# Optimization experiments

Hardware: AMD Instinct MI355X
Metric: run time of the kernel (lower is better)

The kernel has to match this reference:

```python
import jax, jax.numpy as jnp
import numpy as np

N = 32768      # nodes
E = 262144     # edges (avg degree 8)
F = 64         # channels per irrep
Z = 10         # species
R = 8          # radial basis size
H = 64         # radial MLP hidden
P_TP = 5       # TP paths: 0x0->0, 0x1->1, 1x0->1, 1x1->0, 1x1->1
P_SC = 9       # symmetric-contraction paths up to correlation 3
EPS = 0.25     # epsilon ~ 1/sqrt(avg_num_neighbors)


def _split(x):
    # [N, 4F] -> scalars [N,F], vectors [N,F,3] (irreps F x (0e + 1o))
    return x[:, :F], x[:, F:].reshape(x.shape[0], F, 3)


def _merge(s, v):
    return jnp.concatenate([s, v.reshape(v.shape[0], 3 * F)], axis=-1)


def _lin(s, v, Ws, Wv):
    # irreps-wise linear (separate channel mixing per l), fan-in normalized
    inv = 1.0 / np.sqrt(F)
    return (s @ Ws) * inv, jnp.einsum('nfc,fg->ngc', v, Wv) * inv


def _linZ(s, v, Ws, Wv, species):
    # per-species indexed linear, extra 1/sqrt(num_species) as in linZ
    inv = 1.0 / np.sqrt(F * Z)
    return (jnp.einsum('nf,nfg->ng', s, Ws[species]) * inv,
            jnp.einsum('nfc,nfg->ngc', v, Wv[species]) * inv)


def setup_inputs() -> dict:
    key = jax.random.key(0)
    ks = jax.random.split(key, 24)
    f32 = jnp.float32
    return {
        'vectors': jax.random.normal(ks[0], (E, 3), f32),
        'node_feats': jax.random.normal(ks[1], (N, 4 * F), f32),
        'radial_embeddings': jax.random.normal(ks[2], (E, R), f32),
        'W_skip_s': jax.random.normal(ks[3], (Z, F, F), f32),
        'W_skip_v': jax.random.normal(ks[4], (Z, F, F), f32),
        'W_up_s': jax.random.normal(ks[5], (F, F), f32),
        'W_up_v': jax.random.normal(ks[6], (F, F), f32),
        'W_mlp1': jax.random.normal(ks[7], (R, H), f32),
        'W_mlp2': jax.random.normal(ks[8], (H, H), f32),
        'W_mlp3': jax.random.normal(ks[9], (H, H), f32),
        'W_mlp4': jax.random.normal(ks[10], (H, P_TP * F), f32),
        'W_down_s': jax.random.normal(ks[11], (F, F), f32),
        'W_down_v': jax.random.normal(ks[12], (F, F), f32),
        'W_sc': jax.random.normal(ks[13], (Z, P_SC, F), f32),
        'W_post_s': jax.random.normal(ks[14], (F, F), f32),
        'W_post_v': jax.random.normal(ks[15], (F, F), f32),
        'W_out': jax.random.normal(ks[16], (F, 1), f32),
        'node_species': jax.random.randint(ks[17], (N,), 0, Z),
        'senders': jax.random.randint(ks[18], (E,), 0, N),
        'receivers': jax.random.randint(ks[19], (E,), 0, N),
    }


def reference(vectors, node_feats, radial_embeddings, W_skip_s, W_skip_v,
              W_up_s, W_up_v, W_mlp1, W_mlp2, W_mlp3, W_mlp4,
              W_down_s, W_down_v, W_sc, W_post_s, W_post_v, W_out,
              node_species, senders, receivers):
    s, v = _split(node_feats)

    # self connection: per-species skip linear (linZ_skip_tp)
    skip_s, skip_v = _linZ(s, v, W_skip_s, W_skip_v, node_species)

    # linear_up
    s, v = _lin(s, v, W_up_s, W_up_v)

    # spherical harmonics of edge vectors (l=0 is constant, l=1 = unit vector)
    Y1 = vectors / (jnp.linalg.norm(vectors, axis=-1, keepdims=True) + 1e-9)  # [E,3]

    # radial MLP (64,64,64,P_TP*F), no bias, fan-in normalized, silu
    act = jax.nn.silu
    h = act(radial_embeddings @ W_mlp1 * (1.0 / np.sqrt(R)))
    h = act(h @ W_mlp2 * (1.0 / np.sqrt(H)))
    h = act(h @ W_mlp3 * (1.0 / np.sqrt(H)))
    w = (h @ W_mlp4 * (1.0 / np.sqrt(H))).reshape(E, P_TP, F)  # per-edge path weights

    # channelwise tensor product: gather senders, CG-couple with Y, scatter to receivers
    ss = s[senders]              # [E,F]
    vv = v[senders]              # [E,F,3]
    dot = jnp.einsum('efc,ec->ef', vv, Y1)        # 1x1 -> 0
    cross = jnp.cross(vv, Y1[:, None, :])         # 1x1 -> 1
    m_s = w[:, 0] * ss + w[:, 3] * dot
    m_v = (w[:, 1][..., None] * Y1[:, None, :]
           + w[:, 2][..., None] * vv
           + w[:, 4][..., None] * cross * (1.0 / np.sqrt(2.0)))
    s = jax.ops.segment_sum(m_s * EPS, receivers, num_segments=N)  # [N,F]
    v = jax.ops.segment_sum(m_v * EPS, receivers, num_segments=N)  # [N,F,3]

    # linear_down
    s, v = _lin(s, v, W_down_s, W_down_v)

    # per-species symmetric contraction, correlation orders 1..3
    wz = W_sc[node_species]             # [N,P_SC,F]
    vn2 = jnp.sum(v * v, axis=-1)       # [N,F] invariant |v|^2
    s_out = (wz[:, 0] * s + wz[:, 1] * s * s + wz[:, 2] * vn2
             + wz[:, 3] * s ** 3 + wz[:, 4] * s * vn2)
    v_out = (wz[:, 5] + wz[:, 6] * s + wz[:, 7] * s * s + wz[:, 8] * vn2)[..., None] * v

    # linear_post_sc + skip connection
    s, v = _lin(s_out, v_out, W_post_s, W_post_v)
    s = s + skip_s
    v = v + skip_v

    # linear_readout to scalar output irreps (0e)
    node_outputs = s @ W_out * (1.0 / np.sqrt(F))  # [N,1]
    return node_outputs, _merge(s, v)
```

## Files before the change

### kernel.cpp

```cpp
#include <hip/hip_runtime.h>
#include <math.h>


#define NN 32768
#define EE 262144
#define EC 131072
#define ZZ 10
#define NB 128
#define NT_MAX 2064
#define INV8 0.125f
#define INV_SQRT8 0.35355339059327373f
#define INVZ 0.039528470752104741f
#define EPS_C 0.25f
#define RS2 0.70710678118654752f

typedef _Float16 f16;
typedef f16 f16x8 __attribute__((ext_vector_type(8)));
typedef f16 f16x4 __attribute__((ext_vector_type(4)));
typedef f16 f16x2 __attribute__((ext_vector_type(2)));
typedef float f32x4 __attribute__((ext_vector_type(4)));

#define LDFRAG(fid) (*(const f16x8*)(fragw + ((size_t)(fid) << 9) + (lane << 3)))

__device__ __forceinline__ unsigned bfpair(float lo, float hi) {
  unsigned ul = __float_as_uint(lo);
  unsigned uh = __float_as_uint(hi);
  ul = (ul + 0x7FFFu + ((ul >> 16) & 1u)) >> 16;
  uh = (uh + 0x7FFFu + ((uh >> 16) & 1u)) >> 16;
  return ul | (uh << 16);
}

__device__ __forceinline__ unsigned short f2h(float x) {
  union { f16 h; unsigned short u; } cv;
  cv.h = (f16)x;
  return cv.u;
}

__device__ __forceinline__ f16x8 pack8(float4 a, float4 b) {
  f16x8 r;
  r[0] = (f16)a.x; r[1] = (f16)a.y; r[2] = (f16)a.z; r[3] = (f16)a.w;
  r[4] = (f16)b.x; r[5] = (f16)b.y; r[6] = (f16)b.z; r[7] = (f16)b.w;
  return r;
}

__device__ __forceinline__ float silu_f(float x) {
  return x / (1.0f + __expf(-x));
}

__global__ __launch_bounds__(256) void k_frag(
    const float* __restrict__ W1, const float* __restrict__ W2,
    const float* __restrict__ W3, const float* __restrict__ W4,
    const float* __restrict__ Wdns, const float* __restrict__ Wdnv,
    const float* __restrict__ Wpss, const float* __restrict__ Wpsv,
    const float* __restrict__ Wsks, const float* __restrict__ Wskv,
    const float* __restrict__ Wups, const float* __restrict__ Wupv,
    unsigned short* __restrict__ fragw) {
  int id = blockIdx.x * 256 + threadIdx.x;
  if (id >= 268 * 64) return;
  int fid = id >> 6, lane = id & 63;
  int q = lane >> 4, c = lane & 15;
  const float* W; int K = 64, N = 64, t, ks; float sc; int w4 = 0;
  if (fid < 4)       { W = W1; K = 8; N = 64; t = fid; ks = 0; sc = INV_SQRT8; }
  else if (fid < 12) { W = W2; t = (fid - 4) >> 1;  ks = (fid - 4) & 1;  sc = INV8; }
  else if (fid < 20) { W = W3; t = (fid - 12) >> 1; ks = (fid - 12) & 1; sc = INV8; }
  else if (fid < 60) { W = W4; N = 320; t = (fid - 20) >> 1; ks = (fid - 20) & 1; sc = INV8; w4 = 1; }
  else {
    int f2 = fid - 60; sc = INV8;
    if (f2 < 8)        { W = Wdns; }
    else if (f2 < 16)  { W = Wdnv; f2 -= 8; }
    else if (f2 < 24)  { W = Wpss; f2 -= 16; }
    else if (f2 < 32)  { W = Wpsv; f2 -= 24; }
    else if (f2 < 112) { f2 -= 32; W = Wsks + (f2 >> 3) * 4096; f2 &= 7; sc = INVZ; }
    else if (f2 < 192) { f2 -= 112; W = Wskv + (f2 >> 3) * 4096; f2 &= 7; sc = INVZ; }
    else if (f2 < 200) { W = Wups; f2 -= 192; }
    else               { W = Wupv; f2 -= 200; }
    t = f2 >> 1; ks = f2 & 1;
  }
  int col = w4 ? ((t % 5) * 64 + 4 * c + (t / 5)) : (t * 16 + c);
  unsigned short o[8];
#pragma unroll
  for (int i = 0; i < 8; ++i) {
    int k = ks * 32 + 8 * q + i;
    float v = (k < K) ? W[k * N + col] * sc : 0.0f;
    o[i] = f2h(v);
  }
  *(uint4*)(fragw + (size_t)id * 8) = *(const uint4*)o;
}

__global__ __launch_bounds__(256) void k_hist(const int* __restrict__ rcv,
                                              int* __restrict__ cnt) {
  int e = blockIdx.x * 256 + threadIdx.x;
  atomicAdd(&cnt[rcv[e]], 1);
}

__global__ __launch_bounds__(1024) void k_scan(const int* __restrict__ cnt,
                                               int* __restrict__ row_start,
                                               int* __restrict__ cursor) {
  __shared__ int tot[1024];
  int t = threadIdx.x;
  int base = t * 32;
  int local[32];
  int s = 0;
#pragma unroll
  for (int i = 0; i < 32; ++i) { local[i] = s; s += cnt[base + i]; }
  tot[t] = s;
  __syncthreads();
  for (int off = 1; off < 1024; off <<= 1) {
    int v = (t >= off) ? tot[t - off] : 0;
    __syncthreads();
    tot[t] += v;
    __syncthreads();
  }
  int prefix = (t == 0) ? 0 : tot[t - 1];
#pragma unroll
  for (int i = 0; i < 32; ++i) {
    int v = prefix + local[i];
    row_start[base + i] = v;
    cursor[base + i] = v;
  }
  if (t == 1023) row_start[NN] = prefix + s;
}

__global__ __launch_bounds__(256) void k_fill(const int* __restrict__ rcv,
                                              int* __restrict__ cursor,
                                              int* __restrict__ elist) {
  int e = blockIdx.x * 256 + threadIdx.x;
  int pos = atomicAdd(&cursor[rcv[e]], 1);
  elist[pos] = e;
}

__global__ __launch_bounds__(256) void k_nhist(const int* __restrict__ species,
                                               int* __restrict__ sbins,
                                               int* __restrict__ bcnt) {
  __shared__ int h[ZZ];
  int t = threadIdx.x;
  if (t < ZZ) h[t] = 0;
  __syncthreads();
  int n = blockIdx.x * 256 + t;
  atomicAdd(&h[species[n]], 1);
  __syncthreads();
  if (t < ZZ) {
    bcnt[blockIdx.x * ZZ + t] = h[t];
    atomicAdd(&sbins[32 + t], h[t]);
  }
}

__global__ __launch_bounds__(256) void k_nscan(int* __restrict__ sbins,
                                               const int* __restrict__ bcnt,
                                               int* __restrict__ bbase,
                                               int* __restrict__ tspec) {
  __shared__ int sb[12];
  int t = threadIdx.x;
  if (t == 0) {
    int off = 0;
    for (int z = 0; z < ZZ; ++z) {
      sb[z] = off;
      off += ((sbins[32 + z] + 15) >> 4) << 4;
    }
    sb[ZZ] = off;
  }
  __syncthreads();
  if (t < ZZ) {
    int run = sb[t];
    for (int b = 0; b < NB; ++b) {
      bbase[b * ZZ + t] = run;
      run += bcnt[b * ZZ + t];
    }
  }
  for (int i = t; i < NT_MAX; i += 256) {
    int base = i * 16, z = -1;
#pragma unroll
    for (int zz = 0; zz < ZZ; ++zz)
      if (base >= sb[zz] && base < sb[zz + 1]) z = zz;
    tspec[i] = z;
  }
}

__global__ __launch_bounds__(256) void k_nfill(const int* __restrict__ species,
                                               const int* __restrict__ bbase,
                                               int* __restrict__ nperm) {
  __shared__ int cur[ZZ];
  int t = threadIdx.x;
  if (t < ZZ) cur[t] = bbase[blockIdx.x * ZZ + t];
  __syncthreads();
  int n = blockIdx.x * 256 + t;
  int pos = atomicAdd(&cur[species[n]], 1);
  nperm[pos] = n;
}

__global__ __launch_bounds__(256) void k_up2(
    const float* __restrict__ nf,
    const unsigned short* __restrict__ fragw,
    unsigned short* __restrict__ s_up, unsigned short* __restrict__ v_up) {
  int lane = threadIdx.x & 63;
  int wv = threadIdx.x >> 6;
  int n0 = (blockIdx.x * 4 + wv) * 16;
  int q = lane >> 4, c = lane & 15;
  const f32x4 zero4 = {0.f, 0.f, 0.f, 0.f};
  const float* nrow = nf + (size_t)(n0 + c) * 256;

  f16x8 aS[2], aX[2], aY[2], aZ[2];
#pragma unroll
  for (int ks = 0; ks < 2; ++ks) {
    int k0 = ks * 32 + 8 * q;
    aS[ks] = pack8(*(const float4*)(nrow + k0), *(const float4*)(nrow + k0 + 4));
    float vb[24];
    const float4* vp = (const float4*)(nrow + 64 + 3 * k0);
#pragma unroll
    for (int j = 0; j < 6; ++j) *(float4*)(vb + 4 * j) = vp[j];
#pragma unroll
    for (int i = 0; i < 8; ++i) {
      aX[ks][i] = (f16)vb[3 * i];
      aY[ks][i] = (f16)vb[3 * i + 1];
      aZ[ks][i] = (f16)vb[3 * i + 2];
    }
  }

  f32x4 os[4], ox[4], oy[4], oz[4];
#pragma unroll
  for (int t = 0; t < 4; ++t)
#pragma unroll
    for (int ks = 0; ks < 2; ++ks) {
      f16x8 bS = LDFRAG(252 + t * 2 + ks);
      f16x8 bV = LDFRAG(260 + t * 2 + ks);
      os[t] = __builtin_amdgcn_mfma_f32_16x16x32_f16(aS[ks], bS, ks ? os[t] : zero4, 0, 0, 0);
      ox[t] = __builtin_amdgcn_mfma_f32_16x16x32_f16(aX[ks], bV, ks ? ox[t] : zero4, 0, 0, 0);
      oy[t] = __builtin_amdgcn_mfma_f32_16x16x32_f16(aY[ks], bV, ks ? oy[t] : zero4, 0, 0, 0);
      oz[t] = __builtin_amdgcn_mfma_f32_16x16x32_f16(aZ[ks], bV, ks ? oz[t] : zero4, 0, 0, 0);
    }

#pragma unroll
  for (int t = 0; t < 4; ++t)
#pragma unroll
    for (int r = 0; r < 4; ++r) {
      int n = n0 + 4 * q + r;
      int ch = 16 * t + c;
      s_up[n * 64 + ch] = f2h(os[t][r]);
      v_up[(n * 3 + 0) * 64 + ch] = f2h(ox[t][r]);
      v_up[(n * 3 + 1) * 64 + ch] = f2h(oy[t][r]);
      v_up[(n * 3 + 2) * 64 + ch] = f2h(oz[t][r]);
    }
}

__global__ __launch_bounds__(256, 4) void k_mlp(
    const float* __restrict__ re, const int* __restrict__ elist,
    const float* __restrict__ vecs, const int* __restrict__ snd,
    const unsigned short* __restrict__ fragw,
    const unsigned short* __restrict__ s_up,
    const unsigned short* __restrict__ v_up,
    unsigned short* __restrict__ wm, int ip0) {
  __shared__ float hs[4][1088];
  int lane = threadIdx.x & 63;
  int wv = threadIdx.x >> 6;
  int q = lane >> 4, c = lane & 15;
  int ipb = ip0 + (blockIdx.x * 4 + wv) * 16;
  float* hw = hs[wv];
  const f32x4 zero4 = {0.f, 0.f, 0.f, 0.f};

  f16x8 a1 = {0, 0, 0, 0, 0, 0, 0, 0};
  if (q == 0) {
    int e = elist[ipb + c];
    const float4* rp = (const float4*)(re + (size_t)e * 8);
    a1 = pack8(rp[0], rp[1]);
  }
  {
    f32x4 acc[4];
#pragma unroll
    for (int t = 0; t < 4; ++t)
      acc[t] = __builtin_amdgcn_mfma_f32_16x16x32_f16(a1, LDFRAG(t), zero4, 0, 0, 0);
#pragma unroll
    for (int t = 0; t < 4; ++t)
#pragma unroll
      for (int r = 0; r < 4; ++r) {
        float x = silu_f(acc[t][r]);
        hw[(4 * q + r) * 68 + ((16 * t + c) ^ (r << 3))] = x;
      }
  }

#pragma unroll
  for (int L = 0; L < 2; ++L) {
    int base = 4 + 8 * L;
    f16x8 af0, af1;
    {
      const float* hp = hw + c * 68 + 8 * (q ^ (c & 3));
      af0 = pack8(*(const float4*)hp, *(const float4*)(hp + 4));
      af1 = pack8(*(const float4*)(hp + 32), *(const float4*)(hp + 36));
    }
    f32x4 acc[4];
#pragma unroll
    for (int t = 0; t < 4; ++t) {
      acc[t] = __builtin_amdgcn_mfma_f32_16x16x32_f16(af0, LDFRAG(base + t * 2), zero4, 0, 0, 0);
      acc[t] = __builtin_amdgcn_mfma_f32_16x16x32_f16(af1, LDFRAG(base + t * 2 + 1), acc[t], 0, 0, 0);
    }
#pragma unroll
    for (int t = 0; t < 4; ++t)
#pragma unroll
      for (int r = 0; r < 4; ++r) {
        float x = silu_f(acc[t][r]);
        hw[(4 * q + r) * 68 + ((16 * t + c) ^ (r << 3))] = x;
      }
  }

  f16x8 a4k0, a4k1;
  {
    const float* hp = hw + c * 68 + 8 * (q ^ (c & 3));
    a4k0 = pack8(*(const float4*)hp, *(const float4*)(hp + 4));
    a4k1 = pack8(*(const float4*)(hp + 32), *(const float4*)(hp + 36));
  }

  int se_[4];
  float Yx[4], Yy[4], Yz[4];
#pragma unroll
  for (int r = 0; r < 4; ++r) {
    int e = elist[ipb + 4 * q + r];
    float ex = vecs[(size_t)e * 3 + 0];
    float ey = vecs[(size_t)e * 3 + 1];
    float ez = vecs[(size_t)e * 3 + 2];
    float rn = 1.0f / (sqrtf(ex * ex + ey * ey + ez * ez) + 1e-9f);
    Yx[r] = ex * rn; Yy[r] = ey * rn; Yz[r] = ez * rn;
    se_[r] = snd[e];
  }

  size_t orow = (size_t)(ipb - ip0);
#pragma unroll 1
  for (int pg = 0; pg < 2; ++pg) {
    f16x2 gs[4], gx[4], gy[4], gz[4];
#pragma unroll
    for (int r = 0; r < 4; ++r) {
      const unsigned short* sr = s_up + (size_t)se_[r] * 64 + 4 * c + 2 * pg;
      const unsigned short* vr = v_up + (size_t)se_[r] * 192 + 4 * c + 2 * pg;
      gs[r] = *(const f16x2*)sr;
      gx[r] = *(const f16x2*)vr;
      gy[r] = *(const f16x2*)(vr + 64);
      gz[r] = *(const f16x2*)(vr + 128);
    }
    float pms[4], pmx[4], pmy[4], pmz[4];
#pragma unroll
    for (int ig2 = 0; ig2 < 2; ++ig2) {
      int ig = 2 * pg + ig2;
      f32x4 o[5];
#pragma unroll
      for (int p = 0; p < 5; ++p) {
        o[p] = __builtin_amdgcn_mfma_f32_16x16x32_f16(
            a4k0, LDFRAG(20 + (ig * 5 + p) * 2 + 0), zero4, 0, 0, 0);
        o[p] = __builtin_amdgcn_mfma_f32_16x16x32_f16(
            a4k1, LDFRAG(20 + (ig * 5 + p) * 2 + 1), o[p], 0, 0, 0);
      }
#pragma unroll
      for (int r = 0; r < 4; ++r) {
        float ss = (float)gs[r][ig2];
        float vx = (float)gx[r][ig2], vy = (float)gy[r][ig2], vz = (float)gz[r][ig2];
        float dt = vx * Yx[r] + vy * Yy[r] + vz * Yz[r];
        float cx = vy * Yz[r] - vz * Yy[r];
        float cy = vz * Yx[r] - vx * Yz[r];
        float cz = vx * Yy[r] - vy * Yx[r];
        float ms = EPS_C * (o[0][r] * ss + o[3][r] * dt);
        float mx = EPS_C * (o[1][r] * Yx[r] + o[2][r] * vx + o[4][r] * (cx * RS2));
        float my = EPS_C * (o[1][r] * Yy[r] + o[2][r] * vy + o[4][r] * (cy * RS2));
        float mz = EPS_C * (o[1][r] * Yz[r] + o[2][r] * vz + o[4][r] * (cz * RS2));
        if (ig2 == 0) {
          pms[r] = ms; pmx[r] = mx; pmy[r] = my; pmz[r] = mz;
        } else {
          unsigned short* wr = wm + (orow + 4 * q + r) * 256 + 4 * c + 2 * pg;
          *(unsigned*)(wr)       = bfpair(pms[r], ms);
          *(unsigned*)(wr + 64)  = bfpair(pmx[r], mx);
          *(unsigned*)(wr + 128) = bfpair(pmy[r], my);
          *(unsigned*)(wr + 192) = bfpair(pmz[r], mz);
        }
      }
    }
  }
}

__global__ __launch_bounds__(256) void k_gather(
    const unsigned short* __restrict__ m_buf,
    const int* __restrict__ row_start,
    float* __restrict__ acc, int e0, int e1) {
  int g = threadIdx.x & 63;
  int wv = threadIdx.x >> 6;
  int n = blockIdx.x * 4 + wv;
  int beg = row_start[n], end = row_start[n + 1];
  int lo = beg > e0 ? beg : e0;
  int hi = end < e1 ? end : e1;
  if (lo >= hi) return;
  float4 a = make_float4(0.f, 0.f, 0.f, 0.f);
  for (int i = lo; i < hi; ++i) {
    uint2 m = *(const uint2*)(m_buf + (size_t)(i - e0) * 256 + g * 4);
    a.x += __uint_as_float(m.x << 16);
    a.y += __uint_as_float(m.x & 0xFFFF0000u);
    a.z += __uint_as_float(m.y << 16);
    a.w += __uint_as_float(m.y & 0xFFFF0000u);
  }
  float* dst = acc + (size_t)n * 256 + g * 4;
  float4 p = *(const float4*)dst;
  *(float4*)dst = make_float4(a.x + p.x, a.y + p.y, a.z + p.z, a.w + p.w);
}

__global__ __launch_bounds__(128) void k_post2(
    const float* __restrict__ nf, const float* __restrict__ acc,
    const unsigned short* __restrict__ fragw,
    const float* __restrict__ Wsc, const float* __restrict__ Wout,
    const int* __restrict__ nperm, const int* __restrict__ tspec,
    float* __restrict__ out) {
  __shared__ float hs[2][2][1088];
  int lane = threadIdx.x & 63;
  int wv = threadIdx.x >> 6;
  int tt = blockIdx.x * 2 + wv;
  int spec = tspec[tt];
  if (spec < 0) return;
  int q = lane >> 4, c = lane & 15;
  float* hw0 = hs[wv][0];
  float* hw1 = hs[wv][1];
  const f32x4 zero4 = {0.f, 0.f, 0.f, 0.f};

  int nA = nperm[tt * 16 + c];
  size_t rowA = (size_t)((nA < 0) ? 0 : nA);
  const float* arow = acc + rowA * 256;
  const float* nrow = nf + rowA * 256;

  f16x8 aS[2], aVX[2], aVY[2], aVZ[2];
  f16x8 kS[2], kX[2], kY[2], kZ[2];
#pragma unroll
  for (int ks = 0; ks < 2; ++ks) {
    int k0 = ks * 32 + 8 * q;
    aS[ks]  = pack8(*(const float4*)(arow + k0),       *(const float4*)(arow + k0 + 4));
    aVX[ks] = pack8(*(const float4*)(arow + 64 + k0),  *(const float4*)(arow + 68 + k0));
    aVY[ks] = pack8(*(const float4*)(arow + 128 + k0), *(const float4*)(arow + 132 + k0));
    aVZ[ks] = pack8(*(const float4*)(arow + 192 + k0), *(const float4*)(arow + 196 + k0));
    kS[ks]  = pack8(*(const float4*)(nrow + k0),       *(const float4*)(nrow + k0 + 4));
    float vb[24];
    const float4* vp = (const float4*)(nrow + 64 + 3 * k0);
#pragma unroll
    for (int j = 0; j < 6; ++j) *(float4*)(vb + 4 * j) = vp[j];
#pragma unroll
    for (int i = 0; i < 8; ++i) {
      kX[ks][i] = (f16)vb[3 * i];
      kY[ks][i] = (f16)vb[3 * i + 1];
      kZ[ks][i] = (f16)vb[3 * i + 2];
    }
  }

  f32x4 ds[4], dvx[4], dvy[4], dvz[4];
#pragma unroll
  for (int t = 0; t < 4; ++t)
#pragma unroll
    for (int ks = 0; ks < 2; ++ks) {
      f16x8 bS = LDFRAG(60 + t * 2 + ks);
      f16x8 bV = LDFRAG(68 + t * 2 + ks);
      ds[t]  = __builtin_amdgcn_mfma_f32_16x16x32_f16(aS[ks],  bS, ks ? ds[t]  : zero4, 0, 0, 0);
      dvx[t] = __builtin_amdgcn_mfma_f32_16x16x32_f16(aVX[ks], bV, ks ? dvx[t] : zero4, 0, 0, 0);
      dvy[t] = __builtin_amdgcn_mfma_f32_16x16x32_f16(aVY[ks], bV, ks ? dvy[t] : zero4, 0, 0, 0);
      dvz[t] = __builtin_amdgcn_mfma_f32_16x16x32_f16(aVZ[ks], bV, ks ? dvz[t] : zero4, 0, 0, 0);
    }

  f32x4 ps[4], pvx[4], pvy[4], pvz[4];
#pragma unroll
  for (int t = 0; t < 4; ++t)
#pragma unroll
    for (int ks = 0; ks < 2; ++ks) {
      f16x8 bs = LDFRAG(92 + spec * 8 + t * 2 + ks);
      f16x8 bv = LDFRAG(172 + spec * 8 + t * 2 + ks);
      ps[t]  = __builtin_amdgcn_mfma_f32_16x16x32_f16(kS[ks], bs, ks ? ps[t]  : zero4, 0, 0, 0);
      pvx[t] = __builtin_amdgcn_mfma_f32_16x16x32_f16(kX[ks], bv, ks ? pvx[t] : zero4, 0, 0, 0);
      pvy[t] = __builtin_amdgcn_mfma_f32_16x16x32_f16(kY[ks], bv, ks ? pvy[t] : zero4, 0, 0, 0);
      pvz[t] = __builtin_amdgcn_mfma_f32_16x16x32_f16(kZ[ks], bv, ks ? pvz[t] : zero4, 0, 0, 0);
    }

  f32x4 so[4], vcm[4];
  const float* wzp = Wsc + spec * 576 + c;
#pragma unroll
  for (int t = 0; t < 4; ++t) {
    int col = 16 * t;
    float w0 = wzp[col], w1 = wzp[64 + col], w2 = wzp[128 + col];
    float w3 = wzp[192 + col], w4 = wzp[256 + col];
    float w5 = wzp[320 + col], w6 = wzp[384 + col];
    float w7 = wzp[448 + col], w8 = wzp[512 + col];
#pragma unroll
    for (int r = 0; r < 4; ++r) {
      float s = ds[t][r];
      float vx = dvx[t][r], vy = dvy[t][r], vz = dvz[t][r];
      float vn2 = vx * vx + vy * vy + vz * vz;
      so[t][r]  = w0 * s + w1 * s * s + w2 * vn2 + w3 * s * s * s + w4 * s * vn2;
      vcm[t][r] = w5 + w6 * s + w7 * s * s + w8 * vn2;
    }
  }

#pragma unroll
  for (int t = 0; t < 4; ++t)
#pragma unroll
    for (int r = 0; r < 4; ++r) {
      int ad = (4 * q + r) * 68 + ((16 * t + c) ^ (r << 3));
      hw0[ad] = so[t][r];
      hw1[ad] = vcm[t][r] * dvx[t][r];
    }
  {
    f16x8 aP0[2], aP1[2];
#pragma unroll
    for (int ks = 0; ks < 2; ++ks) {
      const float* hp0 = hw0 + c * 68 + ks * 32 + 8 * (q ^ (c & 3));
      const float* hp1 = hw1 + c * 68 + ks * 32 + 8 * (q ^ (c & 3));
      aP0[ks] = pack8(*(const float4*)hp0, *(const float4*)(hp0 + 4));
      aP1[ks] = pack8(*(const float4*)hp1, *(const float4*)(hp1 + 4));
    }
#pragma unroll
    for (int t = 0; t < 4; ++t)
#pragma unroll
      for (int ks = 0; ks < 2; ++ks) {
        ps[t]  = __builtin_amdgcn_mfma_f32_16x16x32_f16(aP0[ks], LDFRAG(76 + t * 2 + ks), ps[t], 0, 0, 0);
        pvx[t] = __builtin_amdgcn_mfma_f32_16x16x32_f16(aP1[ks], LDFRAG(84 + t * 2 + ks), pvx[t], 0, 0, 0);
      }
  }
#pragma unroll
  for (int t = 0; t < 4; ++t)
#pragma unroll
    for (int r = 0; r < 4; ++r) {
      int ad = (4 * q + r) * 68 + ((16 * t + c) ^ (r << 3));
      hw0[ad] = vcm[t][r] * dvy[t][r];
      hw1[ad] = vcm[t][r] * dvz[t][r];
    }
  {
    f16x8 aP0[2], aP1[2];
#pragma unroll
    for (int ks = 0; ks < 2; ++ks) {
      const float* hp0 = hw0 + c * 68 + ks * 32 + 8 * (q ^ (c & 3));
      const float* hp1 = hw1 + c * 68 + ks * 32 + 8 * (q ^ (c & 3));
      aP0[ks] = pack8(*(const float4*)hp0, *(const float4*)(hp0 + 4));
      aP1[ks] = pack8(*(const float4*)hp1, *(const float4*)(hp1 + 4));
    }
#pragma unroll
    for (int t = 0; t < 4; ++t)
#pragma unroll
      for (int ks = 0; ks < 2; ++ks) {
        pvy[t] = __builtin_amdgcn_mfma_f32_16x16x32_f16(aP0[ks], LDFRAG(84 + t * 2 + ks), pvy[t], 0, 0, 0);
        pvz[t] = __builtin_amdgcn_mfma_f32_16x16x32_f16(aP1[ks], LDFRAG(84 + t * 2 + ks), pvz[t], 0, 0, 0);
      }
  }

  float wo[4];
#pragma unroll
  for (int t = 0; t < 4; ++t) wo[t] = Wout[16 * t + c];
  int nst[4];
#pragma unroll
  for (int r = 0; r < 4; ++r) nst[r] = nperm[tt * 16 + 4 * q + r];
#pragma unroll
  for (int r = 0; r < 4; ++r) {
    float part = 0.f;
#pragma unroll
    for (int t = 0; t < 4; ++t) part += ps[t][r] * wo[t];
    part += __shfl_xor(part, 1);
    part += __shfl_xor(part, 2);
    part += __shfl_xor(part, 4);
    part += __shfl_xor(part, 8);
    int n = nst[r];
    if (n >= 0) {
      float* orow = out + NN + (size_t)n * 256;
#pragma unroll
      for (int t = 0; t < 4; ++t) {
        int col = 16 * t + c;
        orow[col] = ps[t][r];
        orow[64 + col * 3 + 0] = pvx[t][r];
        orow[64 + col * 3 + 1] = pvy[t][r];
        orow[64 + col * 3 + 2] = pvz[t][r];
      }
      if (c == 0) out[n] = part * INV8;
    }
  }
}

extern "C" void kernel_launch(void* const* d_in, const int* in_sizes, int n_in,
                              void* d_out, int out_size, void* d_ws, size_t ws_size,
                              hipStream_t stream) {
  (void)in_sizes; (void)n_in; (void)out_size; (void)ws_size;
  const float* vecs = (const float*)d_in[0];
  const float* nf   = (const float*)d_in[1];
  const float* re   = (const float*)d_in[2];
  const float* Wsks = (const float*)d_in[3];
  const float* Wskv = (const float*)d_in[4];
  const float* Wups = (const float*)d_in[5];
  const float* Wupv = (const float*)d_in[6];
  const float* W1   = (const float*)d_in[7];
  const float* W2   = (const float*)d_in[8];
  const float* W3   = (const float*)d_in[9];
  const float* W4   = (const float*)d_in[10];
  const float* Wdns = (const float*)d_in[11];
  const float* Wdnv = (const float*)d_in[12];
  const float* Wsc  = (const float*)d_in[13];
  const float* Wpss = (const float*)d_in[14];
  const float* Wpsv = (const float*)d_in[15];
  const float* Wout = (const float*)d_in[16];
  const int* species = (const int*)d_in[17];
  const int* snd     = (const int*)d_in[18];
  const int* rcv     = (const int*)d_in[19];

  float* ws = (float*)d_ws;
  unsigned short* s_up  = (unsigned short*)ws;
  unsigned short* v_up  = (unsigned short*)(ws + 1048576);
  float* acc   = ws + 4194304;
  unsigned short* fragw = (unsigned short*)(ws + 12582912);
  int* row_st  = (int*)(ws + 12651520);
  int* cursor  = (int*)(ws + 12684352);
  int* elist   = (int*)(ws + 12717120);
  int* nperm   = (int*)(ws + 12979264);
  int* tspec   = (int*)(ws + 13012544);
  int* sbins   = (int*)(ws + 13014848);
  int* bcnt    = (int*)(ws + 13014912);
  int* bbase   = (int*)(ws + 13016192);
  unsigned short* wm = (unsigned short*)(ws + 13017472);

  hipMemsetAsync(cursor, 0, NN * sizeof(int), stream);
  hipMemsetAsync(acc, 0, (size_t)NN * 256 * sizeof(float), stream);
  hipMemsetAsync(sbins, 0, 64 * sizeof(int), stream);
  hipMemsetAsync(nperm, 0xFF, NT_MAX * 16 * sizeof(int), stream);
  k_frag<<<67, 256, 0, stream>>>(W1, W2, W3, W4, Wdns, Wdnv, Wpss, Wpsv,
                                 Wsks, Wskv, Wups, Wupv, fragw);
  k_hist<<<EE / 256, 256, 0, stream>>>(rcv, cursor);
  k_scan<<<1, 1024, 0, stream>>>(cursor, row_st, cursor);
  k_fill<<<EE / 256, 256, 0, stream>>>(rcv, cursor, elist);
  k_nhist<<<NB, 256, 0, stream>>>(species, sbins, bcnt);
  k_nscan<<<1, 256, 0, stream>>>(sbins, bcnt, bbase, tspec);
  k_nfill<<<NB, 256, 0, stream>>>(species, bbase, nperm);
  k_up2<<<512, 256, 0, stream>>>(nf, fragw, s_up, v_up);
  for (int c = 0; c < 2; ++c) {
    k_mlp<<<EC / 64, 256, 0, stream>>>(re, elist, vecs, snd, fragw,
                                       s_up, v_up, wm, c * EC);
    k_gather<<<NN / 4, 256, 0, stream>>>(wm, row_st, acc, c * EC, (c + 1) * EC);
  }
  k_post2<<<NT_MAX / 2, 128, 0, stream>>>(nf, acc, fragw, Wsc, Wout,
                                          nperm, tspec, (float*)d_out);
}
```

Before: 377.6 us.

## Fuse message scatter into edge MLP kernel with float atomics

```diff
diff --git a/kernel.cpp b/kernel.cpp
--- a/kernel.cpp
+++ b/kernel.cpp
@@ -4,7 +4,6 @@
 
 #define NN 32768
 #define EE 262144
-#define EC 131072
 #define ZZ 10
 #define NB 128
 #define NT_MAX 2064
@@ -21,14 +20,6 @@
 typedef float f32x4 __attribute__((ext_vector_type(4)));
 
 #define LDFRAG(fid) (*(const f16x8*)(fragw + ((size_t)(fid) << 9) + (lane << 3)))
-
-__device__ __forceinline__ unsigned bfpair(float lo, float hi) {
-  unsigned ul = __float_as_uint(lo);
-  unsigned uh = __float_as_uint(hi);
-  ul = (ul + 0x7FFFu + ((ul >> 16) & 1u)) >> 16;
-  uh = (uh + 0x7FFFu + ((uh >> 16) & 1u)) >> 16;
-  return ul | (uh << 16);
-}
 
 __device__ __forceinline__ unsigned short f2h(float x) {
   union { f16 h; unsigned short u; } cv;
@@ -245,15 +236,16 @@
 __global__ __launch_bounds__(256, 4) void k_mlp(
     const float* __restrict__ re, const int* __restrict__ elist,
     const float* __restrict__ vecs, const int* __restrict__ snd,
+    const int* __restrict__ rcv,
     const unsigned short* __restrict__ fragw,
     const unsigned short* __restrict__ s_up,
     const unsigned short* __restrict__ v_up,
-    unsigned short* __restrict__ wm, int ip0) {
+    float* __restrict__ acc) {
   __shared__ float hs[4][1088];
   int lane = threadIdx.x & 63;
   int wv = threadIdx.x >> 6;
   int q = lane >> 4, c = lane & 15;
-  int ipb = ip0 + (blockIdx.x * 4 + wv) * 16;
+  int ipb = (blockIdx.x * 4 + wv) * 16;
   float* hw = hs[wv];
   const f32x4 zero4 = {0.f, 0.f, 0.f, 0.f};
 
@@ -264,15 +256,15 @@
     a1 = pack8(rp[0], rp[1]);
   }
   {
-    f32x4 acc[4];
+    f32x4 acr[4];
 #pragma unroll
     for (int t = 0; t < 4; ++t)
-      acc[t] = __builtin_amdgcn_mfma_f32_16x16x32_f16(a1, LDFRAG(t), zero4, 0, 0, 0);
+      acr[t] = __builtin_amdgcn_mfma_f32_16x16x32_f16(a1, LDFRAG(t), zero4, 0, 0, 0);
 #pragma unroll
     for (int t = 0; t < 4; ++t)
 #pragma unroll
       for (int r = 0; r < 4; ++r) {
-        float x = silu_f(acc[t][r]);
+        float x = silu_f(acr[t][r]);
         hw[(4 * q + r) * 68 + ((16 * t + c) ^ (r << 3))] = x;
       }
   }
@@ -286,17 +278,17 @@
       af0 = pack8(*(const float4*)hp, *(const float4*)(hp + 4));
       af1 = pack8(*(const float4*)(hp + 32), *(const float4*)(hp + 36));
     }
-    f32x4 acc[4];
+    f32x4 acr[4];
 #pragma unroll
     for (int t = 0; t < 4; ++t) {
-      acc[t] = __builtin_amdgcn_mfma_f32_16x16x32_f16(af0, LDFRAG(base + t * 2), zero4, 0, 0, 0);
-      acc[t] = __builtin_amdgcn_mfma_f32_16x16x32_f16(af1, LDFRAG(base + t * 2 + 1), acc[t], 0, 0, 0);
+      acr[t] = __builtin_amdgcn_mfma_f32_16x16x32_f16(af0, LDFRAG(base + t * 2), zero4, 0, 0, 0);
+      acr[t] = __builtin_amdgcn_mfma_f32_16x16x32_f16(af1, LDFRAG(base + t * 2 + 1), acr[t], 0, 0, 0);
     }
 #pragma unroll
     for (int t = 0; t < 4; ++t)
 #pragma unroll
       for (int r = 0; r < 4; ++r) {
-        float x = silu_f(acc[t][r]);
+        float x = silu_f(acr[t][r]);
         hw[(4 * q + r) * 68 + ((16 * t + c) ^ (r << 3))] = x;
       }
   }
@@ -308,7 +300,7 @@
     a4k1 = pack8(*(const float4*)(hp + 32), *(const float4*)(hp + 36));
   }
 
-  int se_[4];
+  int se_[4], rv_[4];
   float Yx[4], Yy[4], Yz[4];
 #pragma unroll
   for (int r = 0; r < 4; ++r) {
@@ -319,9 +311,9 @@
     float rn = 1.0f / (sqrtf(ex * ex + ey * ey + ez * ez) + 1e-9f);
     Yx[r] = ex * rn; Yy[r] = ey * rn; Yz[r] = ez * rn;
     se_[r] = snd[e];
-  }
-
-  size_t orow = (size_t)(ipb - ip0);
+    rv_[r] = rcv[e];
+  }
+
 #pragma unroll 1
   for (int pg = 0; pg < 2; ++pg) {
     f16x2 gs[4], gx[4], gy[4], gz[4];
@@ -334,7 +326,6 @@
       gy[r] = *(const f16x2*)(vr + 64);
       gz[r] = *(const f16x2*)(vr + 128);
     }
-    float pms[4], pmx[4], pmy[4], pmz[4];
 #pragma unroll
     for (int ig2 = 0; ig2 < 2; ++ig2) {
       int ig = 2 * pg + ig2;
@@ -358,42 +349,14 @@
         float mx = EPS_C * (o[1][r] * Yx[r] + o[2][r] * vx + o[4][r] * (cx * RS2));
         float my = EPS_C * (o[1][r] * Yy[r] + o[2][r] * vy + o[4][r] * (cy * RS2));
         float mz = EPS_C * (o[1][r] * Yz[r] + o[2][r] * vz + o[4][r] * (cz * RS2));
-        if (ig2 == 0) {
-          pms[r] = ms; pmx[r] = mx; pmy[r] = my; pmz[r] = mz;
-        } else {
-          unsigned short* wr = wm + (orow + 4 * q + r) * 256 + 4 * c + 2 * pg;
-          *(unsigned*)(wr)       = bfpair(pms[r], ms);
-          *(unsigned*)(wr + 64)  = bfpair(pmx[r], mx);
-          *(unsigned*)(wr + 128) = bfpair(pmy[r], my);
-          *(unsigned*)(wr + 192) = bfpair(pmz[r], mz);
-        }
-      }
-    }
-  }
-}
-
-__global__ __launch_bounds__(256) void k_gather(
-    const unsigned short* __restrict__ m_buf,
-    const int* __restrict__ row_start,
-    float* __restrict__ acc, int e0, int e1) {
-  int g = threadIdx.x & 63;
-  int wv = threadIdx.x >> 6;
-  int n = blockIdx.x * 4 + wv;
-  int beg = row_start[n], end = row_start[n + 1];
-  int lo = beg > e0 ? beg : e0;
-  int hi = end < e1 ? end : e1;
-  if (lo >= hi) return;
-  float4 a = make_float4(0.f, 0.f, 0.f, 0.f);
-  for (int i = lo; i < hi; ++i) {
-    uint2 m = *(const uint2*)(m_buf + (size_t)(i - e0) * 256 + g * 4);
-    a.x += __uint_as_float(m.x << 16);
-    a.y += __uint_as_float(m.x & 0xFFFF0000u);
-    a.z += __uint_as_float(m.y << 16);
-    a.w += __uint_as_float(m.y & 0xFFFF0000u);
-  }
-  float* dst = acc + (size_t)n * 256 + g * 4;
-  float4 p = *(const float4*)dst;
-  *(float4*)dst = make_float4(a.x + p.x, a.y + p.y, a.z + p.z, a.w + p.w);
+        float* ap = acc + (size_t)rv_[r] * 256 + 4 * c + 2 * pg + ig2;
+        atomicAdd(ap, ms);
+        atomicAdd(ap + 64, mx);
+        atomicAdd(ap + 128, my);
+        atomicAdd(ap + 192, mz);
+      }
+    }
+  }
 }
 
 __global__ __launch_bounds__(128) void k_post2(
@@ -605,7 +568,6 @@
   int* sbins   = (int*)(ws + 13014848);
   int* bcnt    = (int*)(ws + 13014912);
   int* bbase   = (int*)(ws + 13016192);
-  unsigned short* wm = (unsigned short*)(ws + 13017472);
 
   hipMemsetAsync(cursor, 0, NN * sizeof(int), stream);
   hipMemsetAsync(acc, 0, (size_t)NN * 256 * sizeof(float), stream);
@@ -620,11 +582,8 @@
   k_nscan<<<1, 256, 0, stream>>>(sbins, bcnt, bbase, tspec);
   k_nfill<<<NB, 256, 0, stream>>>(species, bbase, nperm);
   k_up2<<<512, 256, 0, stream>>>(nf, fragw, s_up, v_up);
-  for (int c = 0; c < 2; ++c) {
-    k_mlp<<<EC / 64, 256, 0, stream>>>(re, elist, vecs, snd, fragw,
-                                       s_up, v_up, wm, c * EC);
-    k_gather<<<NN / 4, 256, 0, stream>>>(wm, row_st, acc, c * EC, (c + 1) * EC);
-  }
+  k_mlp<<<EE / 64, 256, 0, stream>>>(re, elist, vecs, snd, rcv, fragw,
+                                     s_up, v_up, acc);
   k_post2<<<NT_MAX / 2, 128, 0, stream>>>(nf, acc, fragw, Wsc, Wout,
                                           nperm, tspec, (float*)d_out);
 }
```

Result: slower. 1.167 ms (+209.1%).
